# Performance work log

Hardware: AMD Instinct MI355X
Metric: run time of the kernel (lower is better)

Reference implementation:

```python
import jax, jax.numpy as jnp
import numpy as np

W_LEN = 10

def _mlp3(x, W1, b1, W2, b2, W3, b3):
    x = jax.nn.relu(x @ W1 + b1)
    x = jax.nn.relu(x @ W2 + b2)
    return x @ W3 + b3

def _make_params(key):
    ks = jax.random.split(key, 16)
    def lin(k, i, o):
        k1, k2 = jax.random.split(k)
        s = 1.0 / np.sqrt(i)
        return (jax.random.uniform(k1, (i, o), jnp.float32, -s, s),
                jax.random.uniform(k2, (o,), jnp.float32, -s, s))
    p = {}
    # encoder: (obs+act)*W = 400 -> 64 -> 64 -> 2
    p['enc_W1'], p['enc_b1'] = lin(ks[0], 400, 64)
    p['enc_W2'], p['enc_b2'] = lin(ks[1], 64, 64)
    p['enc_W3'], p['enc_b3'] = lin(ks[2], 64, 2)
    # GRUCell: input = action+stoch = 10, hidden = det = 2; gates r,z,n
    s = 1.0 / np.sqrt(2)
    p['gru_Wih'] = jax.random.uniform(ks[3], (10, 6), jnp.float32, -s, s)
    p['gru_Whh'] = jax.random.uniform(ks[4], (2, 6), jnp.float32, -s, s)
    p['gru_bih'] = jax.random.uniform(ks[5], (6,), jnp.float32, -s, s)
    p['gru_bhh'] = jax.random.uniform(ks[6], (6,), jnp.float32, -s, s)
    # post_mlp: 2 -> 16 -> 16 -> 2
    p['post_W1'], p['post_b1'] = lin(ks[7], 2, 16)
    p['post_W2'], p['post_b2'] = lin(ks[8], 16, 16)
    p['post_W3'], p['post_b3'] = lin(ks[9], 16, 2)
    # decoder: stoch+action = 10 -> 64 -> 64 -> obs_dim
    p['dec_W1'], p['dec_b1'] = lin(ks[10], 10, 64)
    p['dec_W2'], p['dec_b2'] = lin(ks[11], 64, 64)
    p['dec_W3'], p['dec_b3'] = lin(ks[12], 64, 32)
    return p

def setup_inputs() -> dict:
    key = jax.random.key(0)
    k1, k2, k3, k4, k5 = jax.random.split(key, 5)
    B, T, OD, AD = 512, 512, 32, 8
    N = T - W_LEN + 1
    inp = {
        'obs': jax.random.normal(k1, (B, T, OD), jnp.float32),
        'action': jax.random.normal(k2, (B, T, AD), jnp.float32),
        't_label': jax.random.randint(k3, (B, T), 0, 10, jnp.int32),
        'mask': jax.random.randint(k4, (B, N), 0, 2, jnp.int32),
    }
    inp.update(_make_params(k5))
    return inp

def reference(obs, action, t_label, mask,
              enc_W1, enc_b1, enc_W2, enc_b2, enc_W3, enc_b3,
              gru_Wih, gru_Whh, gru_bih, gru_bhh,
              post_W1, post_b1, post_W2, post_b2, post_W3, post_b3,
              dec_W1, dec_b1, dec_W2, dec_b2, dec_W3, dec_b3):
    B, T, OD = obs.shape
    AD = action.shape[-1]
    N = T - W_LEN + 1
    DET = gru_Whh.shape[0]

    oa = jnp.concatenate([obs, action], axis=-1)            # [B,T,C]
    target_obs_traj = obs[:, W_LEN - 1:, :]                  # [B,N,OD]
    action_traj = action[:, W_LEN - 1:, :]                   # [B,N,AD]
    labels = t_label[:, W_LEN - 1:]

    # torch unfold(1, W, 1): [B,N,C,W] with window along last axis, flatten c-major
    idx = jnp.arange(N)[:, None] + jnp.arange(W_LEN)[None, :]  # [N,W]
    win = oa[:, idx, :]                                      # [B,N,W,C]
    win = jnp.swapaxes(win, 2, 3).reshape(B, N, -1)          # [B,N,C*W]
    priors = _mlp3(win, enc_W1, enc_b1, enc_W2, enc_b2, enc_W3, enc_b3)  # [B,N,S]

    x0 = jnp.zeros((B, DET), obs.dtype)
    s0 = priors[:, 0, :]

    def step(carry, xs):
        x_prev, s_prev = carry
        prior_t, a_t, m_t = xs
        m = m_t[:, None].astype(x_prev.dtype)
        st = m * prior_t + (1.0 - m) * s_prev
        gin = jnp.concatenate([a_t, st], axis=-1)
        gi = gin @ gru_Wih + gru_bih
        gh = x_prev @ gru_Whh + gru_bhh
        ir, iz, inn = jnp.split(gi, 3, axis=-1)
        hr, hz, hn = jnp.split(gh, 3, axis=-1)
        r = jax.nn.sigmoid(ir + hr)
        z = jax.nn.sigmoid(iz + hz)
        n = jnp.tanh(inn + r * hn)
        x_new = (1.0 - z) * n + z * x_prev
        s_new = _mlp3(x_new, post_W1, post_b1, post_W2, post_b2, post_W3, post_b3)
        return (x_new, s_new), (x_new, s_new)

    xs = (jnp.swapaxes(priors[:, :N - 1, :], 0, 1),
          jnp.swapaxes(action_traj[:, :N - 1, :], 0, 1),
          jnp.swapaxes(mask[:, :N - 1], 0, 1))
    _, (x_seq, s_seq) = jax.lax.scan(step, (x0, s0), xs)
    x_traj = jnp.concatenate([x0[:, None, :], jnp.swapaxes(x_seq, 0, 1)], axis=1)  # [B,N,DET]
    posts = jnp.concatenate([s0[:, None, :], jnp.swapaxes(s_seq, 0, 1)], axis=1)   # [B,N,S]

    post_obs_pred = _mlp3(jnp.concatenate([posts, action_traj], axis=-1),
                          dec_W1, dec_b1, dec_W2, dec_b2, dec_W3, dec_b3)          # [B,N,OD]
    return (post_obs_pred, priors, posts, x_traj, target_obs_traj, labels)
```

## Files before the change

kernel.cpp:

```cpp
#include <hip/hip_runtime.h>
#include <hip/hip_bf16.h>

namespace {

constexpr int Bb = 512;
constexpr int Tt = 512;
constexpr int OD = 32;
constexpr int AD = 8;
constexpr int WL = 10;
constexpr int Nn = Tt - WL + 1;
constexpr int CH = OD + AD;
constexpr int REC_T = 512;

constexpr float LOG2E = 1.4426950408889634f;

constexpr long SZ_PO = (long)Bb * Nn * 32;
constexpr long SZ_PR = (long)Bb * Nn * 2;
constexpr long OFF_POST   = 0;
constexpr long OFF_PRIORS = SZ_PO;
constexpr long OFF_POSTS  = OFF_PRIORS + SZ_PR;
constexpr long OFF_XTRAJ  = OFF_POSTS + SZ_PR;
constexpr long OFF_TGT    = OFF_XTRAJ + SZ_PR;
constexpr long OFF_LAB    = OFF_TGT + SZ_PO;

constexpr int PK_W1  = 0;
constexpr int PK_W2  = 26624;
constexpr int PK_W3  = 30720;
constexpr int PK_DW1 = 31744;
constexpr int PK_DW2 = 33792;
constexpr int PK_DW3 = 37888;
constexpr int PK_TOTAL = 39936;

typedef __attribute__((ext_vector_type(8))) short bf16x8;
typedef __attribute__((ext_vector_type(4))) float f32x4;

__device__ __align__(16) short g_pack[PK_TOTAL];

__device__ __forceinline__ f32x4 mfma16(bf16x8 a, bf16x8 b, f32x4 c) {
  return __builtin_amdgcn_mfma_f32_16x16x32_bf16(a, b, c, 0, 0, 0);
}

__device__ __forceinline__ unsigned short f2bf(float x) {
  unsigned int u = __float_as_uint(x);
  unsigned int r = u + 0x7fffu + ((u >> 16) & 1u);
  return (unsigned short)(r >> 16);
}

__device__ __forceinline__ float sigmoidf_(float x) {
  return 1.0f / (1.0f + __expf(-x));
}
__device__ __forceinline__ float tanh_(float x) {
  return 1.0f - 2.0f / (__expf(2.0f * x) + 1.0f);
}

template <int CTRL>
__device__ __forceinline__ float dpp_add(float x) {
  int y = __builtin_amdgcn_update_dpp(0, __float_as_int(x), CTRL, 0xf, 0xf, false);
  return x + __int_as_float(y);
}
template <int CTRL>
__device__ __forceinline__ float dpp_mov(float x) {
  return __int_as_float(
      __builtin_amdgcn_update_dpp(0, __float_as_int(x), CTRL, 0xf, 0xf, false));
}
__device__ __forceinline__ float row16_allsum(float x) {
  x = dpp_add<0xB1>(x);
  x = dpp_add<0x4E>(x);
  x = dpp_add<0x141>(x);
  x = dpp_add<0x140>(x);
  return x;
}

__global__ __launch_bounds__(256) void pack_kernel(
    const float* __restrict__ W1, const float* __restrict__ W2,
    const float* __restrict__ W3, const float* __restrict__ dW1,
    const float* __restrict__ dW2, const float* __restrict__ dW3) {
  const int idx = blockIdx.x * 256 + threadIdx.x;
  if (idx >= PK_TOTAL) return;
  float v = 0.0f;
  int base, r;
  if (idx < PK_W2) {
    base = PK_W1; r = idx - base;
    const int frag = r >> 9, inner = r & 511;
    const int lane = inner >> 3, j = inner & 7;
    const int kb = frag >> 2, jb = frag & 3;
    const int col = lane & 15;
    const int kp = kb * 32 + ((lane >> 4) << 3) + j;
    if (kp < 400) {
      const int w = kp / 40, c = kp - w * 40;
      v = W1[(c * 10 + w) * 64 + jb * 16 + col];
    }
  } else if (idx < PK_W3) {
    base = PK_W2; r = idx - base;
    const int frag = r >> 9, inner = r & 511;
    const int lane = inner >> 3, j = inner & 7;
    const int kb = frag >> 2, jb = frag & 3;
    const int col = lane & 15;
    const int k = kb * 32 + ((lane >> 4) << 3) + j;
    v = W2[k * 64 + jb * 16 + col];
  } else if (idx < PK_DW1) {
    base = PK_W3; r = idx - base;
    const int frag = r >> 9, inner = r & 511;
    const int lane = inner >> 3, j = inner & 7;
    const int kb = frag;
    const int col = lane & 15;
    const int k = kb * 32 + ((lane >> 4) << 3) + j;
    v = (col < 2) ? W3[k * 2 + col] : 0.0f;
  } else if (idx < PK_DW2) {
    base = PK_DW1; r = idx - base;
    const int frag = r >> 9, inner = r & 511;
    const int lane = inner >> 3, j = inner & 7;
    const int jb = frag;
    const int col = lane & 15;
    const int k = ((lane >> 4) << 3) + j;
    v = (k < 10) ? dW1[k * 64 + jb * 16 + col] : 0.0f;
  } else if (idx < PK_DW3) {
    base = PK_DW2; r = idx - base;
    const int frag = r >> 9, inner = r & 511;
    const int lane = inner >> 3, j = inner & 7;
    const int kb = frag >> 2, jb = frag & 3;
    const int col = lane & 15;
    const int k = kb * 32 + ((lane >> 4) << 3) + j;
    v = dW2[k * 64 + jb * 16 + col];
  } else {
    base = PK_DW3; r = idx - base;
    const int frag = r >> 9, inner = r & 511;
    const int lane = inner >> 3, j = inner & 7;
    const int kb = frag >> 1, jb = frag & 1;
    const int col = lane & 15;
    const int k = kb * 32 + ((lane >> 4) << 3) + j;
    v = dW3[k * 32 + jb * 16 + col];
  }
  g_pack[idx] = (short)f2bf(v);
}

__global__ void copy_kernel(const float* __restrict__ obs,
                            const int* __restrict__ tlab,
                            float* __restrict__ out) {
  const int total4 = (int)(SZ_PO / 4);
  const int totalL = Bb * Nn;
  const int stride = gridDim.x * blockDim.x;
  float4* out4 = reinterpret_cast<float4*>(out + OFF_TGT);
  const float4* obs4 = reinterpret_cast<const float4*>(obs);
  for (int idx = blockIdx.x * blockDim.x + threadIdx.x;
       idx < total4 + totalL; idx += stride) {
    if (idx < total4) {
      const int b = idx / (Nn * 8);
      const int r = idx - b * (Nn * 8);
      const int n = r >> 3;
      const int c4 = r & 7;
      out4[idx] = obs4[((long)b * Tt + n + WL - 1) * 8 + c4];
    } else {
      const int j = idx - total4;
      const int b = j / Nn;
      const int n = j - b * Nn;
      out[OFF_LAB + j] = (float)tlab[(long)b * Tt + n + WL - 1];
    }
  }
}

__global__ __launch_bounds__(256) void enc_mfma(
    const float* __restrict__ obs, const float* __restrict__ act,
    const float* __restrict__ b1, const float* __restrict__ b2,
    const float* __restrict__ b3, float* __restrict__ out) {
  __shared__ __align__(16) unsigned short sA[74 * 40];
  __shared__ __align__(16) unsigned short sH1[64 * 64];
  __shared__ __align__(16) unsigned short sH2[64 * 64];
  const int b = blockIdx.x >> 3;
  const int n0 = (blockIdx.x & 7) << 6;
  const int tid = threadIdx.x;
  const int lane = tid & 63, wv = tid >> 6;
  const int q = lane >> 4, lr = lane & 15;
  const int nl = wv * 16 + lr;

  for (int e = tid; e < 74 * 40; e += 256) {
    const int row = e / 40, c = e - row * 40;
    int t = n0 + row; t = t < Tt ? t : Tt - 1;
    const float v = (c < OD) ? obs[((long)b * Tt + t) * OD + c]
                             : act[((long)b * Tt + t) * AD + c - OD];
    sA[e] = f2bf(v);
  }
  __syncthreads();

  const char* sAb = (const char*)sA;
  f32x4 acc[4] = {{0,0,0,0},{0,0,0,0},{0,0,0,0},{0,0,0,0}};
  {
    int c0 = q * 8, w = 0;
#pragma unroll
    for (int kb = 0; kb < 13; ++kb) {
      const bf16x8 a = *(const bf16x8*)(sAb + (nl + w) * 80 + c0 * 2);
#pragma unroll
      for (int jb = 0; jb < 4; ++jb) {
        const bf16x8 bw =
            *(const bf16x8*)&g_pack[PK_W1 + ((kb * 4 + jb) * 64 + lane) * 8];
        acc[jb] = mfma16(a, bw, acc[jb]);
      }
      c0 += 32;
      if (c0 >= 40) { c0 -= 40; ++w; }
    }
  }
  {
#pragma unroll
    for (int jb = 0; jb < 4; ++jb) {
      const float bb = b1[jb * 16 + lr];
#pragma unroll
      for (int r = 0; r < 4; ++r) {
        const int grow = wv * 16 + q * 4 + r;
        const int col = jb * 16 + lr;
        const float v = fmaxf(acc[jb][r] + bb, 0.0f);
        const int byte = (grow * 128 + col * 2) ^ ((grow & 7) << 4);
        *(unsigned short*)((char*)sH1 + byte) = f2bf(v);
      }
    }
  }
  __syncthreads();

  f32x4 ac2[4] = {{0,0,0,0},{0,0,0,0},{0,0,0,0},{0,0,0,0}};
#pragma unroll
  for (int kb = 0; kb < 2; ++kb) {
    const int byte = (nl * 128 + kb * 64 + q * 16) ^ ((lr & 7) << 4);
    const bf16x8 a = *(const bf16x8*)((const char*)sH1 + byte);
#pragma unroll
    for (int jb = 0; jb < 4; ++jb) {
      const bf16x8 bw =
          *(const bf16x8*)&g_pack[PK_W2 + ((kb * 4 + jb) * 64 + lane) * 8];
      ac2[jb] = mfma16(a, bw, ac2[jb]);
    }
  }
  {
#pragma unroll
    for (int jb = 0; jb < 4; ++jb) {
      const float bb = b2[jb * 16 + lr];
#pragma unroll
      for (int r = 0; r < 4; ++r) {
        const int grow = wv * 16 + q * 4 + r;
        const int col = jb * 16 + lr;
        const float v = fmaxf(ac2[jb][r] + bb, 0.0f);
        const int byte = (grow * 128 + col * 2) ^ ((grow & 7) << 4);
        *(unsigned short*)((char*)sH2 + byte) = f2bf(v);
      }
    }
  }
  __syncthreads();

  f32x4 ac3 = {0, 0, 0, 0};
#pragma unroll
  for (int kb = 0; kb < 2; ++kb) {
    const int byte = (nl * 128 + kb * 64 + q * 16) ^ ((lr & 7) << 4);
    const bf16x8 a = *(const bf16x8*)((const char*)sH2 + byte);
    const bf16x8 bw = *(const bf16x8*)&g_pack[PK_W3 + (kb * 64 + lane) * 8];
    ac3 = mfma16(a, bw, ac3);
  }
  if (lr < 2) {
    const float bb = b3[lr];
#pragma unroll
    for (int r = 0; r < 4; ++r) {
      const int grow = wv * 16 + q * 4 + r;
      const int n = n0 + grow;
      if (n < Nn) out[OFF_PRIORS + ((long)b * Nn + n) * 2 + lr] = ac3[r] + bb;
    }
  }
}

__global__ __launch_bounds__(256) void dec_mfma(
    const float* __restrict__ act, const float* __restrict__ b1,
    const float* __restrict__ b2, const float* __restrict__ b3,
    float* __restrict__ out) {
  __shared__ __align__(16) unsigned short sD[64 * 32];
  __shared__ __align__(16) unsigned short sH1[64 * 64];
  __shared__ __align__(16) unsigned short sH2[64 * 64];
  const int b = blockIdx.x >> 3;
  const int n0 = (blockIdx.x & 7) << 6;
  const int tid = threadIdx.x;
  const int lane = tid & 63, wv = tid >> 6;
  const int q = lane >> 4, lr = lane & 15;
  const int nl = wv * 16 + lr;
  const float* posts = out + OFF_POSTS;

  for (int e = tid; e < 64 * 32; e += 256) {
    const int row = e >> 5, c = e & 31;
    int n = n0 + row; n = n < Nn ? n : Nn - 1;
    float v = 0.0f;
    if (c < 2) v = posts[((long)b * Nn + n) * 2 + c];
    else if (c < 10) v = act[((long)b * Tt + n + WL - 1) * AD + c - 2];
    const int byte = (row * 64 + c * 2) ^ ((row & 3) << 4);
    *(unsigned short*)((char*)sD + byte) = f2bf(v);
  }
  __syncthreads();

  f32x4 acc[4] = {{0,0,0,0},{0,0,0,0},{0,0,0,0},{0,0,0,0}};
  {
    const int byte = (nl * 64 + q * 16) ^ ((nl & 3) << 4);
    const bf16x8 a = *(const bf16x8*)((const char*)sD + byte);
#pragma unroll
    for (int jb = 0; jb < 4; ++jb) {
      const bf16x8 bw = *(const bf16x8*)&g_pack[PK_DW1 + (jb * 64 + lane) * 8];
      acc[jb] = mfma16(a, bw, acc[jb]);
    }
  }
  {
#pragma unroll
    for (int jb = 0; jb < 4; ++jb) {
      const float bb = b1[jb * 16 + lr];
#pragma unroll
      for (int r = 0; r < 4; ++r) {
        const int grow = wv * 16 + q * 4 + r;
        const int col = jb * 16 + lr;
        const float v = fmaxf(acc[jb][r] + bb, 0.0f);
        const int byte = (grow * 128 + col * 2) ^ ((grow & 7) << 4);
        *(unsigned short*)((char*)sH1 + byte) = f2bf(v);
      }
    }
  }
  __syncthreads();

  f32x4 ac2[4] = {{0,0,0,0},{0,0,0,0},{0,0,0,0},{0,0,0,0}};
#pragma unroll
  for (int kb = 0; kb < 2; ++kb) {
    const int byte = (nl * 128 + kb * 64 + q * 16) ^ ((lr & 7) << 4);
    const bf16x8 a = *(const bf16x8*)((const char*)sH1 + byte);
#pragma unroll
    for (int jb = 0; jb < 4; ++jb) {
      const bf16x8 bw =
          *(const bf16x8*)&g_pack[PK_DW2 + ((kb * 4 + jb) * 64 + lane) * 8];
      ac2[jb] = mfma16(a, bw, ac2[jb]);
    }
  }
  {
#pragma unroll
    for (int jb = 0; jb < 4; ++jb) {
      const float bb = b2[jb * 16 + lr];
#pragma unroll
      for (int r = 0; r < 4; ++r) {
        const int grow = wv * 16 + q * 4 + r;
        const int col = jb * 16 + lr;
        const float v = fmaxf(ac2[jb][r] + bb, 0.0f);
        const int byte = (grow * 128 + col * 2) ^ ((grow & 7) << 4);
        *(unsigned short*)((char*)sH2 + byte) = f2bf(v);
      }
    }
  }
  __syncthreads();

  f32x4 ac3[2] = {{0,0,0,0},{0,0,0,0}};
#pragma unroll
  for (int kb = 0; kb < 2; ++kb) {
    const int byte = (nl * 128 + kb * 64 + q * 16) ^ ((lr & 7) << 4);
    const bf16x8 a = *(const bf16x8*)((const char*)sH2 + byte);
#pragma unroll
    for (int jb = 0; jb < 2; ++jb) {
      const bf16x8 bw =
          *(const bf16x8*)&g_pack[PK_DW3 + ((kb * 2 + jb) * 64 + lane) * 8];
      ac3[jb] = mfma16(a, bw, ac3[jb]);
    }
  }
#pragma unroll
  for (int jb = 0; jb < 2; ++jb) {
    const int o = jb * 16 + lr;
    const float bb = b3[o];
#pragma unroll
    for (int r = 0; r < 4; ++r) {
      const int grow = wv * 16 + q * 4 + r;
      const int n = n0 + grow;
      if (n < Nn) out[OFF_POST + ((long)b * Nn + n) * 32 + o] = ac3[jb][r] + bb;
    }
  }
}

__global__ __launch_bounds__(256) void gprep_kernel(
    const float* __restrict__ act, const int* __restrict__ mask,
    const float* __restrict__ Wih, const float* __restrict__ bih,
    const float* __restrict__ out, float* __restrict__ rec) {
  const int idx = blockIdx.x * 256 + threadIdx.x;
  const int total = Bb * REC_T;
  if (idx >= total) return;
  const int sub = idx & 3;
  const int t = (idx >> 2) & (REC_T - 1);
  const int blk = idx >> 11;
  const int g = (blk << 2) + sub;
  const float sc[6] = {-LOG2E, -LOG2E, -LOG2E, -LOG2E, 2.f * LOG2E, 2.f * LOG2E};
  float r[12];
#pragma unroll
  for (int i = 0; i < 12; ++i) r[i] = 0.0f;
  if (t < Nn - 1) {
    const float* a = act + ((long)g * Tt + WL - 1 + t) * AD;
    const float4 a0 = *reinterpret_cast<const float4*>(a);
    const float4 a1 = *reinterpret_cast<const float4*>(a + 4);
#pragma unroll
    for (int q = 0; q < 6; ++q) {
      float acc = bih[q];
      acc = fmaf(a0.x, Wih[0 * 6 + q], acc);
      acc = fmaf(a0.y, Wih[1 * 6 + q], acc);
      acc = fmaf(a0.z, Wih[2 * 6 + q], acc);
      acc = fmaf(a0.w, Wih[3 * 6 + q], acc);
      acc = fmaf(a1.x, Wih[4 * 6 + q], acc);
      acc = fmaf(a1.y, Wih[5 * 6 + q], acc);
      acc = fmaf(a1.z, Wih[6 * 6 + q], acc);
      acc = fmaf(a1.w, Wih[7 * 6 + q], acc);
      r[q] = acc * sc[q];
    }
    const float2 pr =
        *reinterpret_cast<const float2*>(out + OFF_PRIORS + ((long)g * Nn + t) * 2);
    r[6] = pr.x;
    r[7] = pr.y;
    r[8] = (float)mask[(long)g * Nn + t];
  }
  float4* o = reinterpret_cast<float4*>(rec + (long)idx * 12);
  o[0] = make_float4(r[0], r[1], r[2], r[3]);
  o[1] = make_float4(r[4], r[5], r[6], r[7]);
  o[2] = make_float4(r[8], r[9], r[10], r[11]);
}

#define SCAN_STEP(GA, GB, MF, TG)                                           \
  do {                                                                      \
    const bool mm = ((MF) != 0.0f);                                         \
    const float st0 = mm ? (GB).z : s0p;                                    \
    const float st1 = mm ? (GB).w : s1p;                                    \
    float giq[6], ghq[6];                                                   \
    _Pragma("unroll") for (int q_ = 0; q_ < 6; ++q_) ghq[q_] =              \
        fmaf(x1p, whh1[q_], fmaf(x0p, whh0[q_], bhhv[q_]));                 \
    giq[0] = fmaf(st1, wih9[0], fmaf(st0, wih8[0], (GA).x));                \
    giq[1] = fmaf(st1, wih9[1], fmaf(st0, wih8[1], (GA).y));                \
    giq[2] = fmaf(st1, wih9[2], fmaf(st0, wih8[2], (GA).z));                \
    giq[3] = fmaf(st1, wih9[3], fmaf(st0, wih8[3], (GA).w));                \
    giq[4] = fmaf(st1, wih9[4], fmaf(st0, wih8[4], (GB).x));                \
    giq[5] = fmaf(st1, wih9[5], fmaf(st0, wih8[5], (GB).y));                \
    const float e0 = __builtin_amdgcn_exp2f(giq[0] + ghq[0]);               \
    const float e1 = __builtin_amdgcn_exp2f(giq[1] + ghq[1]);               \
    const float e2 = __builtin_amdgcn_exp2f(giq[2] + ghq[2]);               \
    const float e3 = __builtin_amdgcn_exp2f(giq[3] + ghq[3]);               \
    const float r0 = __builtin_amdgcn_rcpf(1.0f + e0);                      \
    const float r1 = __builtin_amdgcn_rcpf(1.0f + e1);                      \
    const float z0 = __builtin_amdgcn_rcpf(1.0f + e2);                      \
    const float z1 = __builtin_amdgcn_rcpf(1.0f + e3);                      \
    const float en0 = __builtin_amdgcn_exp2f(fmaf(r0, ghq[4], giq[4]));     \
    const float en1 = __builtin_amdgcn_exp2f(fmaf(r1, ghq[5], giq[5]));     \
    const float nn0 = fmaf(-2.0f, __builtin_amdgcn_rcpf(1.0f + en0), 1.0f); \
    const float nn1 = fmaf(-2.0f, __builtin_amdgcn_rcpf(1.0f + en1), 1.0f); \
    const float xn0 = fmaf(z0, x0p - nn0, nn0);                             \
    const float xn1 = fmaf(z1, x1p - nn1, nn1);                             \
    const float h1 = fmaxf(fmaf(xn1, w1c1, fmaf(xn0, w1c0, b1v)), 0.0f);    \
    const float t0 = h1;                                                    \
    const float t1 = dpp_mov<0xB1>(t0);                                     \
    const float t2 = dpp_mov<0x4E>(t0);                                     \
    const float t3 = dpp_mov<0x4E>(t1);                                     \
    const float t4 = dpp_mov<0x141>(t0);                                    \
    const float t5 = dpp_mov<0x141>(t1);                                    \
    const float t6 = dpp_mov<0x141>(t2);                                    \
    const float t7 = dpp_mov<0x141>(t3);                                    \
    const float t8 = dpp_mov<0x128>(t0);                                    \
    const float t9 = dpp_mov<0x128>(t1);                                    \
    const float t10 = dpp_mov<0x128>(t2);                                   \
    const float t11 = dpp_mov<0x128>(t3);                                   \
    const float t12 = dpp_mov<0x128>(t4);                                   \
    const float t13 = dpp_mov<0x128>(t5);                                   \
    const float t14 = dpp_mov<0x128>(t6);                                   \
    const float t15 = dpp_mov<0x128>(t7);                                   \
    float q0 = fmaf(t0, wg[0], b2v);                                        \
    q0 = fmaf(t1, wg[1], q0);                                               \
    q0 = fmaf(t2, wg[2], q0);                                               \
    q0 = fmaf(t3, wg[3], q0);                                               \
    float q1 = t4 * wg[4];                                                  \
    q1 = fmaf(t5, wg[5], q1);                                               \
    q1 = fmaf(t6, wg[6], q1);                                               \
    q1 = fmaf(t7, wg[7], q1);                                               \
    float q2 = t8 * wg[8];                                                  \
    q2 = fmaf(t9, wg[9], q2);                                               \
    q2 = fmaf(t10, wg[10], q2);                                             \
    q2 = fmaf(t11, wg[11], q2);                                             \
    float q3 = t12 * wg[12];                                                \
    q3 = fmaf(t13, wg[13], q3);                                             \
    q3 = fmaf(t14, wg[14], q3);                                             \
    q3 = fmaf(t15, wg[15], q3);                                             \
    const float h2 = fmaxf((q0 + q1) + (q2 + q3), 0.0f);                    \
    float p0 = row16_allsum(h2 * w3a);                                      \
    float p1 = row16_allsum(h2 * w3b);                                      \
    const float sn0 = p0 + b3a;                                             \
    const float sn1 = p1 + b3b;                                             \
    if (lane == 0 && (TG) < Nn - 1)                                         \
      *reinterpret_cast<float2*>(xw) = make_float2(xn0, xn1);               \
    if (lane == 1 && (TG) < Nn - 1)                                         \
      *reinterpret_cast<float2*>(sw) = make_float2(sn0, sn1);               \
    xw += 2;                                                                \
    sw += 2;                                                                \
    x0p = xn0;                                                              \
    x1p = xn1;                                                              \
    s0p = sn0;                                                              \
    s1p = sn1;                                                              \
  } while (0)

#define LOADCH(C)                                                     \
  do {                                                                \
    const float* p_ = gsrc + (C) * 768 + tid * 12;                    \
    st0 = *reinterpret_cast<const float4*>(p_);                       \
    st1 = *reinterpret_cast<const float4*>(p_ + 4);                   \
    st2 = *reinterpret_cast<const float4*>(p_ + 8);                   \
  } while (0)
#define WRITECH(BUF)                                                  \
  do {                                                                \
    float* q_ = &slds[BUF][tid * 12];                                 \
    *reinterpret_cast<float4*>(q_) = st0;                             \
    *reinterpret_cast<float4*>(q_ + 4) = st1;                         \
    *reinterpret_cast<float4*>(q_ + 8) = st2;                         \
  } while (0)

__global__ __launch_bounds__(64, 1) void scan4_kernel(
    const float* __restrict__ rec, const float* __restrict__ pW2,
    const float* __restrict__ pW1, const float* __restrict__ pb1,
    const float* __restrict__ pb2, const float* __restrict__ pW3,
    const float* __restrict__ pb3, const float* __restrict__ Wih,
    const float* __restrict__ Whh, const float* __restrict__ bhh,
    const float* __restrict__ obs, const int* __restrict__ tlab,
    float* __restrict__ out) {
  __shared__ __align__(16) float slds[2][768];
  const int tid = threadIdx.x;

  if (blockIdx.x >= 128) {
    const int total4 = (int)(SZ_PO / 4);
    const int totalL = Bb * Nn;
    const int stride = (gridDim.x - 128) * 64;
    float4* out4 = reinterpret_cast<float4*>(out + OFF_TGT);
    const float4* obs4 = reinterpret_cast<const float4*>(obs);
    for (int idx = (blockIdx.x - 128) * 64 + tid; idx < total4 + totalL;
         idx += stride) {
      if (idx < total4) {
        const int b = idx / (Nn * 8);
        const int r = idx - b * (Nn * 8);
        const int n = r >> 3;
        const int c4 = r & 7;
        out4[idx] = obs4[((long)b * Tt + n + WL - 1) * 8 + c4];
      } else {
        const int j = idx - total4;
        const int b = j / Nn;
        const int n = j - b * Nn;
        out[OFF_LAB + j] = (float)tlab[(long)b * Tt + n + WL - 1];
      }
    }
    return;
  }

  const int lane = tid & 15;
  const int sub = tid >> 4;
  const int blk = blockIdx.x;
  const int g = (blk << 2) + sub;

  const float sc[6] = {-LOG2E, -LOG2E, -LOG2E, -LOG2E, 2.f * LOG2E, 2.f * LOG2E};
  float wih8[6], wih9[6], whh0[6], whh1[6], bhhv[6];
#pragma unroll
  for (int q = 0; q < 6; ++q) {
    wih8[q] = Wih[8 * 6 + q] * sc[q];
    wih9[q] = Wih[9 * 6 + q] * sc[q];
    whh0[q] = Whh[q] * sc[q];
    whh1[q] = Whh[6 + q] * sc[q];
    bhhv[q] = bhh[q] * sc[q];
  }
  const float w1c0 = pW1[lane], w1c1 = pW1[16 + lane], b1v = pb1[lane];
  constexpr int otab[16] = {0, 1, 2, 3, 7, 6, 5, 4, 8, 9, 10, 11, 15, 14, 13, 12};
  float wg[16];
#pragma unroll
  for (int i = 0; i < 16; ++i) wg[i] = pW2[(lane ^ otab[i]) * 16 + lane];
  const float b2v = pb2[lane];
  const float w3a = pW3[lane * 2], w3b = pW3[lane * 2 + 1];
  const float b3a = pb3[0], b3b = pb3[1];

  const float* priors = out + OFF_PRIORS;
  const long pbase = (long)g * Nn;
  const float* gsrc = rec + (long)blk * (REC_T * 48);
  float* xw = out + OFF_XTRAJ + pbase * 2 + 2;
  float* sw = out + OFF_POSTS + pbase * 2 + 2;

  const float2 s0v = *reinterpret_cast<const float2*>(priors + pbase * 2);
  float x0p = 0.f, x1p = 0.f;
  float s0p = s0v.x, s1p = s0v.y;
  if (lane == 0)
    *reinterpret_cast<float2*>(out + OFF_XTRAJ + pbase * 2) =
        make_float2(0.f, 0.f);
  if (lane == 1)
    *reinterpret_cast<float2*>(out + OFF_POSTS + pbase * 2) =
        make_float2(s0p, s1p);

  float4 st0, st1, st2;
  LOADCH(0);
  WRITECH(0);
  LOADCH(1);

  float4 cGA, cGB;
  float cMF;
  {
    const float* rp = &slds[0][(sub)*12];
    cGA = *reinterpret_cast<const float4*>(rp);
    cGB = *reinterpret_cast<const float4*>(rp + 4);
    cMF = rp[8];
  }

  int tg = 0;
  for (int c = 0; c < 32; ++c) {
    const int buf = c & 1;
    if (c + 1 < 32) WRITECH((c + 1) & 1);
    if (c + 2 < 32) LOADCH(c + 2);
#pragma unroll
    for (int tl = 0; tl < 16; ++tl) {
      const float4 GA = cGA;
      const float4 GB = cGB;
      const float MF = cMF;
      const int ntl = (tl + 1) & 15;
      const int nbuf = (tl == 15) ? (buf ^ 1) : buf;
      const float* rp = &slds[nbuf][(ntl * 4 + sub) * 12];
      cGA = *reinterpret_cast<const float4*>(rp);
      cGB = *reinterpret_cast<const float4*>(rp + 4);
      cMF = rp[8];
      SCAN_STEP(GA, GB, MF, tg);
      ++tg;
    }
  }
}

__global__ __launch_bounds__(64) void scan_fb_kernel(
    const float* __restrict__ act, const int* __restrict__ mask,
    const float* __restrict__ Wih, const float* __restrict__ Whh,
    const float* __restrict__ bih, const float* __restrict__ bhh,
    const float* __restrict__ pW1, const float* __restrict__ pb1,
    const float* __restrict__ pW2, const float* __restrict__ pb2,
    const float* __restrict__ pW3, const float* __restrict__ pb3,
    float* __restrict__ out) {
  const int tid = threadIdx.x;
  const int lane = tid & 15;
  const int g = (blockIdx.x * 64 + tid) >> 4;

  float wih8[6], wih9[6], whh0[6], whh1[6], bhhv[6], bihv[6];
  float wihA[8][6];
#pragma unroll
  for (int q = 0; q < 6; ++q) {
    wih8[q] = Wih[8 * 6 + q];
    wih9[q] = Wih[9 * 6 + q];
    whh0[q] = Whh[q];
    whh1[q] = Whh[6 + q];
    bhhv[q] = bhh[q];
    bihv[q] = bih[q];
  }
#pragma unroll
  for (int i = 0; i < 8; ++i)
#pragma unroll
    for (int q = 0; q < 6; ++q) wihA[i][q] = Wih[i * 6 + q];

  const float w1c0 = pW1[lane], w1c1 = pW1[16 + lane], b1v = pb1[lane];
  float w2c[16];
#pragma unroll
  for (int k = 0; k < 16; ++k) w2c[k] = pW2[k * 16 + lane];
  const float b2v = pb2[lane];
  const float w3a = pW3[lane * 2], w3b = pW3[lane * 2 + 1];
  const float b3a = pb3[0], b3b = pb3[1];

  const float* priors = out + OFF_PRIORS;
  float* posts = out + OFF_POSTS;
  float* xtraj = out + OFF_XTRAJ;
  const long pbase = (long)g * Nn;
  const float* aptr = act + ((long)g * Tt + WL - 1) * 8;

  const float2 s0v = *reinterpret_cast<const float2*>(priors + pbase * 2);
  float x0p = 0.f, x1p = 0.f;
  float s0p = s0v.x, s1p = s0v.y;
  if (lane == 0)
    *reinterpret_cast<float2*>(xtraj + pbase * 2) = make_float2(0.f, 0.f);
  if (lane == 1)
    *reinterpret_cast<float2*>(posts + pbase * 2) = make_float2(s0p, s1p);

  float4 an0 = *reinterpret_cast<const float4*>(aptr);
  float4 an1 = *reinterpret_cast<const float4*>(aptr + 4);
  float2 prn = s0v;
  int mn = mask[pbase];

  for (int t = 0; t < Nn - 1; ++t) {
    const float4 a0 = an0, a1 = an1;
    const float2 pr = prn;
    const int m = mn;
    const int tn1 = (t + 1 < Nn - 1) ? t + 1 : Nn - 2;
    an0 = *reinterpret_cast<const float4*>(aptr + (long)tn1 * 8);
    an1 = *reinterpret_cast<const float4*>(aptr + (long)tn1 * 8 + 4);
    prn = *reinterpret_cast<const float2*>(priors + (pbase + t + 1) * 2);
    mn = mask[pbase + t + 1];

    const float st0 = m ? pr.x : s0p;
    const float st1 = m ? pr.y : s1p;

    float giq[6], ghq[6];
#pragma unroll
    for (int q = 0; q < 6; ++q) {
      float acc = bihv[q];
      acc = fmaf(a0.x, wihA[0][q], acc);
      acc = fmaf(a0.y, wihA[1][q], acc);
      acc = fmaf(a0.z, wihA[2][q], acc);
      acc = fmaf(a0.w, wihA[3][q], acc);
      acc = fmaf(a1.x, wihA[4][q], acc);
      acc = fmaf(a1.y, wihA[5][q], acc);
      acc = fmaf(a1.z, wihA[6][q], acc);
      acc = fmaf(a1.w, wihA[7][q], acc);
      giq[q] = fmaf(st1, wih9[q], fmaf(st0, wih8[q], acc));
      ghq[q] = fmaf(x1p, whh1[q], fmaf(x0p, whh0[q], bhhv[q]));
    }
    const float r0 = sigmoidf_(giq[0] + ghq[0]);
    const float r1 = sigmoidf_(giq[1] + ghq[1]);
    const float z0 = sigmoidf_(giq[2] + ghq[2]);
    const float z1 = sigmoidf_(giq[3] + ghq[3]);
    const float nn0 = tanh_(fmaf(r0, ghq[4], giq[4]));
    const float nn1 = tanh_(fmaf(r1, ghq[5], giq[5]));
    const float xn0 = fmaf(z0, x0p - nn0, nn0);
    const float xn1 = fmaf(z1, x1p - nn1, nn1);

    const float h1 = fmaxf(fmaf(xn1, w1c1, fmaf(xn0, w1c0, b1v)), 0.0f);
    float ha[16];
#pragma unroll
    for (int k = 0; k < 16; ++k) ha[k] = __shfl(h1, k, 16);
    float q0 = fmaf(ha[0], w2c[0], b2v);
    q0 = fmaf(ha[1], w2c[1], q0);
    q0 = fmaf(ha[2], w2c[2], q0);
    q0 = fmaf(ha[3], w2c[3], q0);
    float q1 = ha[4] * w2c[4];
    q1 = fmaf(ha[5], w2c[5], q1);
    q1 = fmaf(ha[6], w2c[6], q1);
    q1 = fmaf(ha[7], w2c[7], q1);
    float q2 = ha[8] * w2c[8];
    q2 = fmaf(ha[9], w2c[9], q2);
    q2 = fmaf(ha[10], w2c[10], q2);
    q2 = fmaf(ha[11], w2c[11], q2);
    float q3 = ha[12] * w2c[12];
    q3 = fmaf(ha[13], w2c[13], q3);
    q3 = fmaf(ha[14], w2c[14], q3);
    q3 = fmaf(ha[15], w2c[15], q3);
    const float h2 = fmaxf((q0 + q1) + (q2 + q3), 0.0f);

    float p0 = row16_allsum(h2 * w3a);
    float p1 = row16_allsum(h2 * w3b);
    const float sn0 = p0 + b3a;
    const float sn1 = p1 + b3b;

    if (lane == 0)
      *reinterpret_cast<float2*>(xtraj + (pbase + t + 1) * 2) =
          make_float2(xn0, xn1);
    if (lane == 1)
      *reinterpret_cast<float2*>(posts + (pbase + t + 1) * 2) =
          make_float2(sn0, sn1);
    x0p = xn0; x1p = xn1; s0p = sn0; s1p = sn1;
  }
}

}

extern "C" void kernel_launch(void* const* d_in, const int* in_sizes, int n_in,
                              void* d_out, int out_size, void* d_ws, size_t ws_size,
                              hipStream_t stream) {
  const float* obs    = (const float*)d_in[0];
  const float* action = (const float*)d_in[1];
  const int* t_label  = (const int*)d_in[2];
  const int* mask     = (const int*)d_in[3];
  const float* enc_W1 = (const float*)d_in[4];
  const float* enc_b1 = (const float*)d_in[5];
  const float* enc_W2 = (const float*)d_in[6];
  const float* enc_b2 = (const float*)d_in[7];
  const float* enc_W3 = (const float*)d_in[8];
  const float* enc_b3 = (const float*)d_in[9];
  const float* gru_Wih = (const float*)d_in[10];
  const float* gru_Whh = (const float*)d_in[11];
  const float* gru_bih = (const float*)d_in[12];
  const float* gru_bhh = (const float*)d_in[13];
  const float* post_W1 = (const float*)d_in[14];
  const float* post_b1 = (const float*)d_in[15];
  const float* post_W2 = (const float*)d_in[16];
  const float* post_b2 = (const float*)d_in[17];
  const float* post_W3 = (const float*)d_in[18];
  const float* post_b3 = (const float*)d_in[19];
  const float* dec_W1 = (const float*)d_in[20];
  const float* dec_b1 = (const float*)d_in[21];
  const float* dec_W2 = (const float*)d_in[22];
  const float* dec_b2 = (const float*)d_in[23];
  const float* dec_W3 = (const float*)d_in[24];
  const float* dec_b3 = (const float*)d_in[25];
  float* out = (float*)d_out;

  pack_kernel<<<(PK_TOTAL + 255) / 256, 256, 0, stream>>>(
      enc_W1, enc_W2, enc_W3, dec_W1, dec_W2, dec_W3);

  enc_mfma<<<Bb * 8, 256, 0, stream>>>(obs, action, enc_b1, enc_b2, enc_b3,
                                       out);

  const size_t rec_bytes = (size_t)Bb * REC_T * 12 * sizeof(float);
  if (ws_size >= rec_bytes) {
    float* rec = (float*)d_ws;
    const int total = Bb * REC_T;
    gprep_kernel<<<(total + 255) / 256, 256, 0, stream>>>(
        action, mask, gru_Wih, gru_bih, out, rec);
    scan4_kernel<<<128 + 2048, 64, 0, stream>>>(
        rec, post_W2, post_W1, post_b1, post_b2, post_W3, post_b3, gru_Wih,
        gru_Whh, gru_bhh, obs, t_label, out);
  } else {
    scan_fb_kernel<<<128, 64, 0, stream>>>(
        action, mask, gru_Wih, gru_Whh, gru_bih, gru_bhh, post_W1, post_b1,
        post_W2, post_b2, post_W3, post_b3, out);
    copy_kernel<<<2048, 256, 0, stream>>>(obs, t_label, out);
  }

  dec_mfma<<<Bb * 8, 256, 0, stream>>>(action, dec_b1, dec_b2, dec_b3, out);
}
```

Before: 240.6 us.

## Fold masked prior into GRU input precompute and pack scan as 1024-thread blocks

The masked prior contribution to the GRU input gates is now precomputed in gprep, so each scan step only multiplies the previous posterior by a (1-mask) factor. This removes the per-step select, and the record shrinks from 12 to 8 floats, cutting workspace traffic and LDS staging. The scan kernel also changes from 128 blocks of 64 threads to 8 blocks of 1024 threads, each wave with its own LDS slice, and the copy work now runs in 248 large blocks. Packing the serial scan waves onto fewer CUs can change per-wave latency and contention on the sequential critical path.

```diff
diff --git a/kernel.cpp b/kernel.cpp
--- a/kernel.cpp
+++ b/kernel.cpp
@@ -376,16 +376,19 @@
   if (idx >= total) return;
   const int sub = idx & 3;
   const int t = (idx >> 2) & (REC_T - 1);
-  const int blk = idx >> 11;
-  const int g = (blk << 2) + sub;
+  const int wgid = idx >> 11;
+  const int g = (wgid << 2) + sub;
   const float sc[6] = {-LOG2E, -LOG2E, -LOG2E, -LOG2E, 2.f * LOG2E, 2.f * LOG2E};
-  float r[12];
-#pragma unroll
-  for (int i = 0; i < 12; ++i) r[i] = 0.0f;
+  float r[8];
+#pragma unroll
+  for (int i = 0; i < 8; ++i) r[i] = 0.0f;
   if (t < Nn - 1) {
     const float* a = act + ((long)g * Tt + WL - 1 + t) * AD;
     const float4 a0 = *reinterpret_cast<const float4*>(a);
     const float4 a1 = *reinterpret_cast<const float4*>(a + 4);
+    const int m = mask[(long)g * Nn + t];
+    const float2 pr =
+        *reinterpret_cast<const float2*>(out + OFF_PRIORS + ((long)g * Nn + t) * 2);
 #pragma unroll
     for (int q = 0; q < 6; ++q) {
       float acc = bih[q];
@@ -397,34 +400,32 @@
       acc = fmaf(a1.y, Wih[5 * 6 + q], acc);
       acc = fmaf(a1.z, Wih[6 * 6 + q], acc);
       acc = fmaf(a1.w, Wih[7 * 6 + q], acc);
+      if (m) {
+        acc = fmaf(pr.x, Wih[8 * 6 + q], acc);
+        acc = fmaf(pr.y, Wih[9 * 6 + q], acc);
+      }
       r[q] = acc * sc[q];
     }
-    const float2 pr =
-        *reinterpret_cast<const float2*>(out + OFF_PRIORS + ((long)g * Nn + t) * 2);
-    r[6] = pr.x;
-    r[7] = pr.y;
-    r[8] = (float)mask[(long)g * Nn + t];
-  }
-  float4* o = reinterpret_cast<float4*>(rec + (long)idx * 12);
+    r[6] = m ? 0.0f : 1.0f;
+  }
+  float4* o = reinterpret_cast<float4*>(rec + (long)idx * 8);
   o[0] = make_float4(r[0], r[1], r[2], r[3]);
   o[1] = make_float4(r[4], r[5], r[6], r[7]);
-  o[2] = make_float4(r[8], r[9], r[10], r[11]);
-}
-
-#define SCAN_STEP(GA, GB, MF, TG)                                           \
+}
+
+#define SCAN_STEP(GA, GB, TG)                                               \
   do {                                                                      \
-    const bool mm = ((MF) != 0.0f);                                         \
-    const float st0 = mm ? (GB).z : s0p;                                    \
-    const float st1 = mm ? (GB).w : s1p;                                    \
+    const float sm0 = (GB).z * s0p;                                         \
+    const float sm1 = (GB).z * s1p;                                         \
     float giq[6], ghq[6];                                                   \
     _Pragma("unroll") for (int q_ = 0; q_ < 6; ++q_) ghq[q_] =              \
         fmaf(x1p, whh1[q_], fmaf(x0p, whh0[q_], bhhv[q_]));                 \
-    giq[0] = fmaf(st1, wih9[0], fmaf(st0, wih8[0], (GA).x));                \
-    giq[1] = fmaf(st1, wih9[1], fmaf(st0, wih8[1], (GA).y));                \
-    giq[2] = fmaf(st1, wih9[2], fmaf(st0, wih8[2], (GA).z));                \
-    giq[3] = fmaf(st1, wih9[3], fmaf(st0, wih8[3], (GA).w));                \
-    giq[4] = fmaf(st1, wih9[4], fmaf(st0, wih8[4], (GB).x));                \
-    giq[5] = fmaf(st1, wih9[5], fmaf(st0, wih8[5], (GB).y));                \
+    giq[0] = fmaf(sm1, wih9[0], fmaf(sm0, wih8[0], (GA).x));                \
+    giq[1] = fmaf(sm1, wih9[1], fmaf(sm0, wih8[1], (GA).y));                \
+    giq[2] = fmaf(sm1, wih9[2], fmaf(sm0, wih8[2], (GA).z));                \
+    giq[3] = fmaf(sm1, wih9[3], fmaf(sm0, wih8[3], (GA).w));                \
+    giq[4] = fmaf(sm1, wih9[4], fmaf(sm0, wih8[4], (GB).x));                \
+    giq[5] = fmaf(sm1, wih9[5], fmaf(sm0, wih8[5], (GB).y));                \
     const float e0 = __builtin_amdgcn_exp2f(giq[0] + ghq[0]);               \
     const float e1 = __builtin_amdgcn_exp2f(giq[1] + ghq[1]);               \
     const float e2 = __builtin_amdgcn_exp2f(giq[2] + ghq[2]);               \
@@ -489,22 +490,10 @@
     s1p = sn1;                                                              \
   } while (0)
 
-#define LOADCH(C)                                                     \
-  do {                                                                \
-    const float* p_ = gsrc + (C) * 768 + tid * 12;                    \
-    st0 = *reinterpret_cast<const float4*>(p_);                       \
-    st1 = *reinterpret_cast<const float4*>(p_ + 4);                   \
-    st2 = *reinterpret_cast<const float4*>(p_ + 8);                   \
-  } while (0)
-#define WRITECH(BUF)                                                  \
-  do {                                                                \
-    float* q_ = &slds[BUF][tid * 12];                                 \
-    *reinterpret_cast<float4*>(q_) = st0;                             \
-    *reinterpret_cast<float4*>(q_ + 4) = st1;                         \
-    *reinterpret_cast<float4*>(q_ + 8) = st2;                         \
-  } while (0)
-
-__global__ __launch_bounds__(64, 1) void scan4_kernel(
+#define LOADCH(C) stg = *reinterpret_cast<const float4*>(gsrc + (C) * 256 + wtid * 4)
+#define WRITECH(BUF) *reinterpret_cast<float4*>(&slds[wv][BUF][wtid * 4]) = stg
+
+__global__ __launch_bounds__(1024, 1) void scan6_kernel(
     const float* __restrict__ rec, const float* __restrict__ pW2,
     const float* __restrict__ pW1, const float* __restrict__ pb1,
     const float* __restrict__ pb2, const float* __restrict__ pW3,
@@ -512,16 +501,16 @@
     const float* __restrict__ Whh, const float* __restrict__ bhh,
     const float* __restrict__ obs, const int* __restrict__ tlab,
     float* __restrict__ out) {
-  __shared__ __align__(16) float slds[2][768];
+  __shared__ __align__(16) float slds[16][2][256];
   const int tid = threadIdx.x;
 
-  if (blockIdx.x >= 128) {
+  if (blockIdx.x >= 8) {
     const int total4 = (int)(SZ_PO / 4);
     const int totalL = Bb * Nn;
-    const int stride = (gridDim.x - 128) * 64;
+    const int stride = (gridDim.x - 8) * 1024;
     float4* out4 = reinterpret_cast<float4*>(out + OFF_TGT);
     const float4* obs4 = reinterpret_cast<const float4*>(obs);
-    for (int idx = (blockIdx.x - 128) * 64 + tid; idx < total4 + totalL;
+    for (int idx = (blockIdx.x - 8) * 1024 + tid; idx < total4 + totalL;
          idx += stride) {
       if (idx < total4) {
         const int b = idx / (Nn * 8);
@@ -539,10 +528,12 @@
     return;
   }
 
-  const int lane = tid & 15;
-  const int sub = tid >> 4;
-  const int blk = blockIdx.x;
-  const int g = (blk << 2) + sub;
+  const int wv = tid >> 6;
+  const int wtid = tid & 63;
+  const int lane = wtid & 15;
+  const int sub = wtid >> 4;
+  const int wgid = blockIdx.x * 16 + wv;
+  const int g = (wgid << 2) + sub;
 
   const float sc[6] = {-LOG2E, -LOG2E, -LOG2E, -LOG2E, 2.f * LOG2E, 2.f * LOG2E};
   float wih8[6], wih9[6], whh0[6], whh1[6], bhhv[6];
@@ -565,7 +556,7 @@
 
   const float* priors = out + OFF_PRIORS;
   const long pbase = (long)g * Nn;
-  const float* gsrc = rec + (long)blk * (REC_T * 48);
+  const float* gsrc = rec + (long)wgid * (REC_T * 32);
   float* xw = out + OFF_XTRAJ + pbase * 2 + 2;
   float* sw = out + OFF_POSTS + pbase * 2 + 2;
 
@@ -579,37 +570,33 @@
     *reinterpret_cast<float2*>(out + OFF_POSTS + pbase * 2) =
         make_float2(s0p, s1p);
 
-  float4 st0, st1, st2;
+  float4 stg;
   LOADCH(0);
   WRITECH(0);
   LOADCH(1);
 
   float4 cGA, cGB;
-  float cMF;
   {
-    const float* rp = &slds[0][(sub)*12];
+    const float* rp = &slds[wv][0][(sub)*8];
     cGA = *reinterpret_cast<const float4*>(rp);
     cGB = *reinterpret_cast<const float4*>(rp + 4);
-    cMF = rp[8];
   }
 
   int tg = 0;
-  for (int c = 0; c < 32; ++c) {
+  for (int c = 0; c < 64; ++c) {
     const int buf = c & 1;
-    if (c + 1 < 32) WRITECH((c + 1) & 1);
-    if (c + 2 < 32) LOADCH(c + 2);
-#pragma unroll
-    for (int tl = 0; tl < 16; ++tl) {
+    if (c + 1 < 64) WRITECH((c + 1) & 1);
+    if (c + 2 < 64) LOADCH(c + 2);
+#pragma unroll
+    for (int tl = 0; tl < 8; ++tl) {
       const float4 GA = cGA;
       const float4 GB = cGB;
-      const float MF = cMF;
-      const int ntl = (tl + 1) & 15;
-      const int nbuf = (tl == 15) ? (buf ^ 1) : buf;
-      const float* rp = &slds[nbuf][(ntl * 4 + sub) * 12];
+      const int ntl = (tl + 1) & 7;
+      const int nbuf = (tl == 7) ? (buf ^ 1) : buf;
+      const float* rp = &slds[wv][nbuf][(ntl * 4 + sub) * 8];
       cGA = *reinterpret_cast<const float4*>(rp);
       cGB = *reinterpret_cast<const float4*>(rp + 4);
-      cMF = rp[8];
-      SCAN_STEP(GA, GB, MF, tg);
+      SCAN_STEP(GA, GB, tg);
       ++tg;
     }
   }
@@ -783,13 +770,13 @@
   enc_mfma<<<Bb * 8, 256, 0, stream>>>(obs, action, enc_b1, enc_b2, enc_b3,
                                        out);
 
-  const size_t rec_bytes = (size_t)Bb * REC_T * 12 * sizeof(float);
+  const size_t rec_bytes = (size_t)Bb * REC_T * 8 * sizeof(float);
   if (ws_size >= rec_bytes) {
     float* rec = (float*)d_ws;
     const int total = Bb * REC_T;
     gprep_kernel<<<(total + 255) / 256, 256, 0, stream>>>(
         action, mask, gru_Wih, gru_bih, out, rec);
-    scan4_kernel<<<128 + 2048, 64, 0, stream>>>(
+    scan6_kernel<<<8 + 248, 1024, 0, stream>>>(
         rec, post_W2, post_W1, post_b1, post_b2, post_W3, post_b3, gru_Wih,
         gru_Whh, gru_bhh, obs, t_label, out);
   } else {
```

Measured after the change: 562.3 us. 134% more time.
